# Optimization experiments

Hardware: AMD Instinct MI355X
Metric: run time of the kernel (lower is better)

The kernel has to match this reference:

```python
import jax, jax.numpy as jnp
import numpy as np
import math

B, S, V = 16, 128, 32000
D_MODEL, D_STATE, L, T = 1024, 512, 2, 4
TAU, THR = 2.0, 1.0
DECAY = math.exp(-1.0 / TAU)  # membrane decay exp(-1/tau)
EPS = 1e-5
ALPHA = 2.0  # ATan surrogate alpha


@jax.custom_vjp
def atan_spike(x):
    # spikingjelly surrogate.ATan: heaviside forward, atan-derivative backward
    return (x >= 0.0).astype(x.dtype)

def _atan_fwd(x):
    return atan_spike(x), x

def _atan_bwd(x, g):
    return (g * (ALPHA / 2.0) / (1.0 + (jnp.pi / 2.0 * ALPHA * x) ** 2),)

atan_spike.defvjp(_atan_fwd, _atan_bwd)


def lif(mem, x):
    # AdaptiveLIFNeuron in eval mode: threshold fixed at base_threshold=1.0
    mem_t = mem * DECAY + x
    spike = atan_spike(mem_t - THR)
    return mem_t * (1.0 - spike), spike  # soft-ish reset: mem*(1-spike)


def layernorm(x, g, b):
    m = jnp.mean(x, -1, keepdims=True)
    v = jnp.mean((x - m) ** 2, -1, keepdims=True)
    return (x - m) * jax.lax.rsqrt(v + EPS) * g + b


def setup_inputs() -> dict:
    key = jax.random.key(0)
    ks = jax.random.split(key, 8)

    def w(k, shape, fan_in):
        return (jax.random.normal(k, shape, jnp.float32) / np.sqrt(fan_in).astype(np.float32))

    return {
        "input_ids": jax.random.randint(ks[0], (B, S), 0, V),
        "emb_table": jax.random.normal(ks[1], (V, D_MODEL), jnp.float32) * 0.02,
        "W_enc": w(ks[2], (D_MODEL, D_MODEL), D_MODEL),
        "b_enc": jnp.zeros((D_MODEL,), jnp.float32),
        "ln_s_g": jnp.ones((L, D_STATE), jnp.float32),
        "ln_s_b": jnp.zeros((L, D_STATE), jnp.float32),
        "Wg": w(ks[3], (L, D_STATE, D_MODEL), D_STATE),
        "bg": jnp.zeros((L, D_MODEL), jnp.float32),
        "ln_e_g": jnp.ones((L, D_MODEL), jnp.float32),
        "ln_e_b": jnp.zeros((L, D_MODEL), jnp.float32),
        "Wi": w(ks[4], (L, D_MODEL, D_STATE), D_MODEL),
        "bi": jnp.zeros((L, D_STATE), jnp.float32),
        "W_out": w(ks[5], (D_STATE, V), D_STATE),
        "b_out": jnp.zeros((V,), jnp.float32),
    }


def reference(input_ids, emb_table, W_enc, b_enc, ln_s_g, ln_s_b, Wg, bg,
              ln_e_g, ln_e_b, Wi, bi, W_out, b_out):
    token_emb = emb_table[input_ids]           # [B,S,D_MODEL]
    emb_seq = jnp.swapaxes(token_emb, 0, 1)    # [S,B,D_MODEL]

    init = (
        jnp.zeros((L, B, D_STATE), jnp.float32),  # top-down states per layer
        jnp.zeros((B, D_MODEL), jnp.float32),      # input-encoder LIF mem
        jnp.zeros((L, B, D_MODEL), jnp.float32),   # generative LIF mems
        jnp.zeros((L, B, D_STATE), jnp.float32),   # inference LIF mems
    )

    def token_step(carry, emb_t):
        states, enc_mem, gen_mems, inf_mems = carry
        # input encoder: Linear + LIF; bottom_up_input is the spike output
        enc_mem, bottom = lif(enc_mem, emb_t @ W_enc + b_enc)
        for _t in range(T):
            for j in range(L):
                s = states[j]
                # generative pathway: prediction from top-down state
                pre = layernorm(s, ln_s_g[j], ln_s_b[j]) @ Wg[j] + bg[j]
                gm, pred = lif(gen_mems[j], pre)
                gen_mems = gen_mems.at[j].set(gm)
                error = bottom - pred
                # inference pathway: state update from prediction error
                inf_in = layernorm(error, ln_e_g[j], ln_e_b[j]) @ Wi[j] + bi[j]
                im, upd = lif(inf_mems[j], inf_in)
                inf_mems = inf_mems.at[j].set(im)
                states = states.at[j].set(s + upd)
                bottom = error  # error propagates upward / across timesteps
        return (states, enc_mem, gen_mems, inf_mems), states[L - 1]

    _, hs = jax.lax.scan(token_step, init, emb_seq)  # [S,B,D_STATE]
    hs = jnp.swapaxes(hs, 0, 1)                      # [B,S,D_STATE]
    return hs @ W_out + b_out                        # logits [B,S,V]
```

## Files before the change

kernel.cpp:

```cpp
#include <hip/hip_runtime.h>
#include <math.h>

#define NWG 256
#define TPB 256

typedef float v4f __attribute__((ext_vector_type(4)));

constexpr int Bn = 16, Sn = 128, Vn = 32000, DMn = 1024, DSn = 512;
constexpr float DECAYc = 0.6065306597126334f;
constexpr float THRc = 1.0f, EPSc = 1e-5f;

constexpr size_t OF_FLAGS  = 0;
constexpr size_t OF_STATES = (size_t)256*4096;
constexpr size_t OF_E0     = OF_STATES + (size_t)2*16*512*4;
constexpr size_t OF_E1     = OF_E0 + (size_t)16*1024*4;
constexpr size_t OF_ENCX   = OF_E1 + (size_t)16*1024*4;
constexpr size_t OF_HS     = OF_ENCX + (size_t)128*16*1024*4;
constexpr size_t OF_WGT    = OF_HS + (size_t)128*16*512*4;
constexpr size_t OF_WIT    = OF_WGT + (size_t)2*1024*512*4;
constexpr size_t INIT_BYTES = OF_E0;

struct SP {
  const int* ids; const float* emb;
  const float* W_enc; const float* b_enc;
  const float* ln_s_g; const float* ln_s_b;
  const float* Wg; const float* bg;
  const float* ln_e_g; const float* ln_e_b;
  const float* Wi; const float* bi;
};

__device__ __forceinline__ float ld_cg(const float* p) {
  return __hip_atomic_load(p, __ATOMIC_RELAXED, __HIP_MEMORY_SCOPE_AGENT);
}
__device__ __forceinline__ void st_cg(float* p, float v) {
  __hip_atomic_store(p, v, __ATOMIC_RELAXED, __HIP_MEMORY_SCOPE_AGENT);
}
__device__ __forceinline__ int ld_flag(const int* p) {
  return __hip_atomic_load(p, __ATOMIC_RELAXED, __HIP_MEMORY_SCOPE_AGENT);
}
__device__ __forceinline__ void st_flag(int* p, int v) {
  __hip_atomic_store(p, v, __ATOMIC_RELAXED, __HIP_MEMORY_SCOPE_AGENT);
}

__device__ __forceinline__ int swc(int c) { return c ^ ((c >> 3) & 7); }

template<int SZ>
__device__ __forceinline__ void bstep(float* v, bool up, int M) {
  #pragma unroll
  for (int q = 0; q < SZ/2; q++) {
    float lo = v[q], hi = v[q + SZ/2];
    float send = up ? lo : hi;
    float recv = __shfl_xor(send, M);
    v[q] = (up ? hi : lo) + recv;
  }
}

template<int K, int NO, int ROP>
__device__ __forceinline__ void step_fn(
    const float* __restrict__ WT,
    const float* __restrict__ bias,
    const float* __restrict__ lng, const float* __restrict__ lnb,
    const float* __restrict__ src,
    float* __restrict__ mreg, float* __restrict__ btreg, float* __restrict__ streg,
    float* __restrict__ encmem, const float* __restrict__ encrow,
    float* __restrict__ errw, float* __restrict__ stw, float* __restrict__ hsw,
    int o0, int grp, float* X, int tid)
{
  constexpr int Kc = K / 64, KC4 = Kc / 4, OPW = NO / 4, NV = 4 * OPW;
  const int w = tid >> 6, l = tid & 63;
  const int o_i   = (OPW == 8) ? ((l >> 3) & 7) : ((l >> 4) & 3);
  const int b_loc = (OPW == 8) ? ((l >> 1) & 3) : ((l >> 2) & 3);
  const int o  = o0 + w*OPW + o_i;
  const int bg = grp*4 + b_loc;

  float eEv = 0.f;
  if (ROP == 1) {
    const float ex = encrow[(size_t)bg*DMn + o];
    const float emt = encmem[0]*DECAYc + ex;
    const float esp = (emt >= THRc) ? 1.f : 0.f;
    encmem[0] = emt * (1.f - esp);
    eEv = esp;
  }

  float wreg[Kc][OPW];
  #pragma unroll
  for (int i = 0; i < OPW; i++) {
    const v4f* wp = (const v4f*)(WT + (size_t)(o0 + w*OPW + i)*K + l*Kc);
    #pragma unroll
    for (int q = 0; q < KC4; q++) {
      v4f v = wp[q];
      #pragma unroll
      for (int e = 0; e < 4; e++) wreg[q*4 + e][i] = v[e];
    }
  }

  {
    v4f xr[KC4];
    const float* sp = src + (size_t)(grp*4 + w)*K + l*Kc;
    #pragma unroll
    for (int q = 0; q < KC4; q++)
      asm volatile("global_load_dwordx4 %0, %1, off sc0 sc1"
                   : "=v"(xr[q]) : "v"(sp + 4*q));
    asm volatile("s_waitcnt vmcnt(0)" ::: "memory");
    __builtin_amdgcn_sched_barrier(0);
    float s1 = 0.f;
    #pragma unroll
    for (int q = 0; q < KC4; q++)
      #pragma unroll
      for (int e = 0; e < 4; e++) s1 += xr[q][e];
    #pragma unroll
    for (int off = 32; off; off >>= 1) s1 += __shfl_xor(s1, off);
    const float mean = s1 * (1.0f / K);
    float s2 = 0.f;
    #pragma unroll
    for (int q = 0; q < KC4; q++)
      #pragma unroll
      for (int e = 0; e < 4; e++) { float d = xr[q][e] - mean; s2 += d*d; }
    #pragma unroll
    for (int off = 32; off; off >>= 1) s2 += __shfl_xor(s2, off);
    const float rstd = 1.0f / sqrtf(s2 * (1.0f / K) + EPSc);
    #pragma unroll
    for (int q = 0; q < KC4; q++) {
      v4f ov;
      #pragma unroll
      for (int e = 0; e < 4; e++) {
        const int k = l*Kc + q*4 + e;
        ov[e] = (xr[q][e] - mean) * rstd * lng[k] + lnb[k];
      }
      *(v4f*)(X + w*K + (swc(l*KC4 + q) << 2)) = ov;
    }
  }
  __syncthreads();

  int xoff[KC4];
  #pragma unroll
  for (int q = 0; q < KC4; q++) xoff[q] = swc(l*KC4 + q) << 2;
  float v[NV];
  #pragma unroll
  for (int n = 0; n < NV; n++) v[n] = 0.f;
  #pragma unroll
  for (int b = 0; b < 4; b++) {
    v4f xv[KC4];
    #pragma unroll
    for (int q = 0; q < KC4; q++) xv[q] = *(const v4f*)(X + b*K + xoff[q]);
    #pragma unroll
    for (int i = 0; i < OPW; i++) {
      float a = v[i*4 + b];
      #pragma unroll
      for (int q = 0; q < KC4; q++)
        #pragma unroll
        for (int e = 0; e < 4; e++) a = fmaf(xv[q][e], wreg[q*4 + e][i], a);
      v[i*4 + b] = a;
    }
  }

  if (OPW == 8) {
    bstep<32>(v, (l & 32) != 0, 32);
    bstep<16>(v, (l & 16) != 0, 16);
    bstep<8> (v, (l &  8) != 0,  8);
    bstep<4> (v, (l &  4) != 0,  4);
    bstep<2> (v, (l &  2) != 0,  2);
    v[0] += __shfl_xor(v[0], 1);
  } else {
    bstep<16>(v, (l & 32) != 0, 32);
    bstep<8> (v, (l & 16) != 0, 16);
    bstep<4> (v, (l &  8) != 0,  8);
    bstep<2> (v, (l &  4) != 0,  4);
    v[0] += __shfl_xor(v[0], 2);
    v[0] += __shfl_xor(v[0], 1);
  }

  const float val = v[0] + bias[o];
  const float mt = mreg[0] * DECAYc + val;
  const float spk = (mt >= THRc) ? 1.f : 0.f;
  mreg[0] = mt * (1.f - spk);
  if (ROP == 1 || ROP == 2) {
    const float ne = ((ROP == 1) ? eEv : btreg[0]) - spk;
    btreg[0] = ne;
    if ((l & 1) == 0) st_cg(errw + (size_t)bg*DMn + o, ne);
  } else {
    const float ns = streg[0] + spk;
    streg[0] = ns;
    if ((l & 3) == 0) {
      st_cg(stw + (size_t)bg*DSn + o, ns);
      if (hsw) hsw[(size_t)bg*DSn + o] = ns;
    }
  }
}

__device__ __forceinline__ void publish(int* myflag, int tid, int epoch) {
  asm volatile("s_waitcnt vmcnt(0)" ::: "memory");
  __syncthreads();
  if (tid == 0) st_flag(myflag, epoch);
}
__device__ __forceinline__ void waithalf(const int* othf, int tid, int target) {
  if (tid < 32) {
    while (ld_flag(othf + tid*1024) < target) { }
  }
  asm volatile("" ::: "memory");
  __syncthreads();
}

__global__ void __launch_bounds__(TPB, 1) snn_scan(SP p, char* __restrict__ ws)
{
  __shared__ float X[21504];
  const int wgg = blockIdx.x, tid = threadIdx.x;
  const int grp = wgg >> 6, wgl = wgg & 63;
  int* flags  = (int*)(ws + OF_FLAGS);
  int* myflag = flags + (size_t)wgg*1024;
  float* states = (float*)(ws + OF_STATES);
  float* e0     = (float*)(ws + OF_E0);
  float* e1     = (float*)(ws + OF_E1);
  const float* encX = (const float*)(ws + OF_ENCX);
  float* hs     = (float*)(ws + OF_HS);
  const float* WgT = (const float*)(ws + OF_WGT);
  const float* WiT = (const float*)(ws + OF_WIT);
  float* ebuf[2] = { e0, e1 };

  if (wgl < 32) {
    const int* othf = flags + (size_t)(grp*64 + 32)*1024;
    float encMem = 0.f, btReg = 0.f, genMem0 = 0.f, genMem1 = 0.f;
    const int o0 = wgl * 32;
    for (int s = 0; s < Sn; s++) {
      for (int it = 0; it < 8; it++) {
        const int j = it & 1;
        waithalf(othf, tid, s*8 + it - 1);
        if (it == 0)
          step_fn<512,32,1>(WgT, p.bg, p.ln_s_g, p.ln_s_b, states,
                            &genMem0, &btReg, nullptr,
                            &encMem, encX + (size_t)s*Bn*DMn,
                            ebuf[0], nullptr, nullptr, o0, grp, X, tid);
        else
          step_fn<512,32,2>(WgT + (size_t)j*DMn*DSn, p.bg + j*DMn,
                            p.ln_s_g + j*DSn, p.ln_s_b + j*DSn,
                            states + (size_t)j*Bn*DSn,
                            j ? &genMem1 : &genMem0, &btReg, nullptr,
                            nullptr, nullptr,
                            ebuf[j], nullptr, nullptr, o0, grp, X, tid);
        publish(myflag, tid, s*8 + it + 1);
      }
    }
  } else {
    const int* othf = flags + (size_t)(grp*64)*1024;
    float infMem0 = 0.f, infMem1 = 0.f, stReg0 = 0.f, stReg1 = 0.f;
    const int o0 = (wgl - 32) * 16;
    for (int s = 0; s < Sn; s++) {
      for (int it = 0; it < 8; it++) {
        const int j = it & 1;
        waithalf(othf, tid, s*8 + it + 1);
        step_fn<1024,16,3>(WiT + (size_t)j*DSn*DMn, p.bi + j*DSn,
                           p.ln_e_g + j*DMn, p.ln_e_b + j*DMn,
                           ebuf[j],
                           j ? &infMem1 : &infMem0, nullptr,
                           j ? &stReg1 : &stReg0,
                           nullptr, nullptr,
                           nullptr, states + (size_t)j*Bn*DSn,
                           (it == 7) ? (hs + (size_t)s*Bn*DSn) : nullptr,
                           o0, grp, X, tid);
        publish(myflag, tid, s*8 + it + 1);
      }
    }
  }
}

__global__ void __launch_bounds__(256) transpose_k(
    const float* __restrict__ in, float* __restrict__ out, int K, int O)
{
  __shared__ float t[32][33];
  const int ob = blockIdx.x * 32, kb = blockIdx.y * 32;
  const int x = threadIdx.x, y = threadIdx.y;
  #pragma unroll
  for (int i = 0; i < 32; i += 8) t[y + i][x] = in[(size_t)(kb + y + i)*O + ob + x];
  __syncthreads();
  #pragma unroll
  for (int i = 0; i < 32; i += 8) out[(size_t)(ob + y + i)*K + kb + x] = t[x][y + i];
}

__global__ void __launch_bounds__(256) enc_gemm(
    const int* __restrict__ ids, const float* __restrict__ emb,
    const float* __restrict__ We, const float* __restrict__ be,
    float* __restrict__ encX)
{
  __shared__ float As[32][128];
  __shared__ float Bs[32][128];
  __shared__ int rowid[128];
  const int tid = threadIdx.x;
  const int ntile = blockIdx.x * 128;
  const int mtile = blockIdx.y * 128;
  if (tid < 128) {
    int m = mtile + tid;
    rowid[tid] = ids[(m & 15)*Sn + (m >> 4)];
  }
  __syncthreads();
  const int tx = tid & 15, ty = tid >> 4;
  float acc[8][8];
  #pragma unroll
  for (int i = 0; i < 8; i++)
    #pragma unroll
    for (int q = 0; q < 8; q++) acc[i][q] = 0.f;

  for (int kb = 0; kb < 32; kb++) {
    #pragma unroll
    for (int r = 0; r < 4; r++) {
      int idx = tid + r*256;
      int m = idx >> 3, kq = idx & 7;
      float4 a = *(const float4*)(emb + (size_t)rowid[m]*DMn + kb*32 + kq*4);
      As[kq*4+0][m] = a.x; As[kq*4+1][m] = a.y;
      As[kq*4+2][m] = a.z; As[kq*4+3][m] = a.w;
    }
    #pragma unroll
    for (int r = 0; r < 4; r++) {
      int idx = tid + r*256;
      int k = idx >> 5, nq = idx & 31;
      *(float4*)(&Bs[k][nq*4]) =
          *(const float4*)(We + (size_t)(kb*32 + k)*DMn + ntile + nq*4);
    }
    __syncthreads();
    #pragma unroll
    for (int k = 0; k < 32; k++) {
      float4 a0 = *(float4*)(&As[k][ty*8]);
      float4 a1 = *(float4*)(&As[k][ty*8+4]);
      float4 b0 = *(float4*)(&Bs[k][tx*8]);
      float4 b1 = *(float4*)(&Bs[k][tx*8+4]);
      float av[8] = {a0.x,a0.y,a0.z,a0.w,a1.x,a1.y,a1.z,a1.w};
      float bv[8] = {b0.x,b0.y,b0.z,b0.w,b1.x,b1.y,b1.z,b1.w};
      #pragma unroll
      for (int i = 0; i < 8; i++)
        #pragma unroll
        for (int q = 0; q < 8; q++) acc[i][q] += av[i]*bv[q];
    }
    __syncthreads();
  }
  const float* bop = be + ntile + tx*8;
  float4 bv0 = *(const float4*)bop;
  float4 bv1 = *(const float4*)(bop + 4);
  #pragma unroll
  for (int i = 0; i < 8; i++) {
    int m = mtile + ty*8 + i;
    float* op = encX + (size_t)m*DMn + ntile + tx*8;
    float4 v0 = make_float4(acc[i][0]+bv0.x, acc[i][1]+bv0.y,
                            acc[i][2]+bv0.z, acc[i][3]+bv0.w);
    float4 v1 = make_float4(acc[i][4]+bv1.x, acc[i][5]+bv1.y,
                            acc[i][6]+bv1.z, acc[i][7]+bv1.w);
    *(float4*)op = v0;
    *(float4*)(op + 4) = v1;
  }
}

__global__ void __launch_bounds__(256) out_gemm(
    const float* __restrict__ hs, const float* __restrict__ Wo,
    const float* __restrict__ bo, float* __restrict__ out)
{
  __shared__ float As[32][128];
  __shared__ float Bs[32][128];
  const int tid = threadIdx.x;
  const int ntile = blockIdx.x * 128;
  const int mtile = blockIdx.y * 128;
  const int tx = tid & 15, ty = tid >> 4;
  float acc[8][8];
  #pragma unroll
  for (int i = 0; i < 8; i++)
    #pragma unroll
    for (int q = 0; q < 8; q++) acc[i][q] = 0.f;

  for (int kb = 0; kb < 16; kb++) {
    #pragma unroll
    for (int r = 0; r < 4; r++) {
      int idx = tid + r*256;
      int m = idx >> 3, kq = idx & 7;
      float4 a = *(const float4*)(hs + (size_t)(mtile + m)*512 + kb*32 + kq*4);
      As[kq*4+0][m] = a.x; As[kq*4+1][m] = a.y;
      As[kq*4+2][m] = a.z; As[kq*4+3][m] = a.w;
    }
    #pragma unroll
    for (int r = 0; r < 4; r++) {
      int idx = tid + r*256;
      int k = idx >> 5, nq = idx & 31;
      *(float4*)(&Bs[k][nq*4]) =
          *(const float4*)(Wo + (size_t)(kb*32 + k)*Vn + ntile + nq*4);
    }
    __syncthreads();
    #pragma unroll
    for (int k = 0; k < 32; k++) {
      float4 a0 = *(float4*)(&As[k][ty*8]);
      float4 a1 = *(float4*)(&As[k][ty*8+4]);
      float4 b0 = *(float4*)(&Bs[k][tx*8]);
      float4 b1 = *(float4*)(&Bs[k][tx*8+4]);
      float av[8] = {a0.x,a0.y,a0.z,a0.w,a1.x,a1.y,a1.z,a1.w};
      float bv[8] = {b0.x,b0.y,b0.z,b0.w,b1.x,b1.y,b1.z,b1.w};
      #pragma unroll
      for (int i = 0; i < 8; i++)
        #pragma unroll
        for (int q = 0; q < 8; q++) acc[i][q] += av[i]*bv[q];
    }
    __syncthreads();
  }
  const float* bop = bo + ntile + tx*8;
  float4 bv0 = *(const float4*)bop;
  float4 bv1 = *(const float4*)(bop + 4);
  #pragma unroll
  for (int i = 0; i < 8; i++) {
    int m = mtile + ty*8 + i;
    float* op = out + ((size_t)(m & 15)*Sn + (m >> 4))*Vn + ntile + tx*8;
    float4 v0 = make_float4(acc[i][0]+bv0.x, acc[i][1]+bv0.y,
                            acc[i][2]+bv0.z, acc[i][3]+bv0.w);
    float4 v1 = make_float4(acc[i][4]+bv1.x, acc[i][5]+bv1.y,
                            acc[i][6]+bv1.z, acc[i][7]+bv1.w);
    *(float4*)op = v0;
    *(float4*)(op + 4) = v1;
  }
}

extern "C" void kernel_launch(void* const* d_in, const int* in_sizes, int n_in,
                              void* d_out, int out_size, void* d_ws, size_t ws_size,
                              hipStream_t stream) {
  (void)in_sizes; (void)n_in; (void)out_size; (void)ws_size;
  SP p;
  p.ids    = (const int*)  d_in[0];
  p.emb    = (const float*)d_in[1];
  p.W_enc  = (const float*)d_in[2];
  p.b_enc  = (const float*)d_in[3];
  p.ln_s_g = (const float*)d_in[4];
  p.ln_s_b = (const float*)d_in[5];
  p.Wg     = (const float*)d_in[6];
  p.bg     = (const float*)d_in[7];
  p.ln_e_g = (const float*)d_in[8];
  p.ln_e_b = (const float*)d_in[9];
  p.Wi     = (const float*)d_in[10];
  p.bi     = (const float*)d_in[11];
  const float* Wo = (const float*)d_in[12];
  const float* bo = (const float*)d_in[13];

  char* ws = (char*)d_ws;
  float* WgT  = (float*)(ws + OF_WGT);
  float* WiT  = (float*)(ws + OF_WIT);
  float* encX = (float*)(ws + OF_ENCX);
  float* hs   = (float*)(ws + OF_HS);

  hipMemsetAsync(ws, 0, INIT_BYTES, stream);

  hipLaunchKernelGGL(transpose_k, dim3(32, 16), dim3(32, 8), 0, stream,
                     p.Wg, WgT, 512, 1024);
  hipLaunchKernelGGL(transpose_k, dim3(32, 16), dim3(32, 8), 0, stream,
                     p.Wg + (size_t)512*1024, WgT + (size_t)1024*512, 512, 1024);
  hipLaunchKernelGGL(transpose_k, dim3(16, 32), dim3(32, 8), 0, stream,
                     p.Wi, WiT, 1024, 512);
  hipLaunchKernelGGL(transpose_k, dim3(16, 32), dim3(32, 8), 0, stream,
                     p.Wi + (size_t)1024*512, WiT + (size_t)512*1024, 1024, 512);

  hipLaunchKernelGGL(enc_gemm, dim3(DMn/128, 2048/128), dim3(256), 0, stream,
                     p.ids, p.emb, p.W_enc, p.b_enc, encX);

  hipLaunchKernelGGL(snn_scan, dim3(NWG), dim3(TPB), 0, stream, p, ws);

  hipLaunchKernelGGL(out_gemm, dim3(Vn/128, 2048/128), dim3(256), 0, stream,
                     hs, Wo, bo, (float*)d_out);
}
```

Baseline: 5.233 ms.

## Keep both layers' weights and layernorm params resident in registers across scan

Before, each step of the persistent scan kernel reloaded its weight slice, layernorm gamma/beta and bias from global memory. Now both layers' slices are loaded once into registers before the sequence loop, and the 8 inner steps are fully unrolled with specialised gen/inf step functions. The aim is to take repeated global weight traffic off the latency-bound serial critical path. The cost is roughly doubled register pressure from holding two layers' weights, which may cause spills. The shared buffer is switched to dynamic allocation of the same size.

```diff
diff --git a/kernel.cpp b/kernel.cpp
--- a/kernel.cpp
+++ b/kernel.cpp
@@ -29,9 +29,6 @@
   const float* Wi; const float* bi;
 };
 
-__device__ __forceinline__ float ld_cg(const float* p) {
-  return __hip_atomic_load(p, __ATOMIC_RELAXED, __HIP_MEMORY_SCOPE_AGENT);
-}
 __device__ __forceinline__ void st_cg(float* p, float v) {
   __hip_atomic_store(p, v, __ATOMIC_RELAXED, __HIP_MEMORY_SCOPE_AGENT);
 }
@@ -55,139 +52,6 @@
   }
 }
 
-template<int K, int NO, int ROP>
-__device__ __forceinline__ void step_fn(
-    const float* __restrict__ WT,
-    const float* __restrict__ bias,
-    const float* __restrict__ lng, const float* __restrict__ lnb,
-    const float* __restrict__ src,
-    float* __restrict__ mreg, float* __restrict__ btreg, float* __restrict__ streg,
-    float* __restrict__ encmem, const float* __restrict__ encrow,
-    float* __restrict__ errw, float* __restrict__ stw, float* __restrict__ hsw,
-    int o0, int grp, float* X, int tid)
-{
-  constexpr int Kc = K / 64, KC4 = Kc / 4, OPW = NO / 4, NV = 4 * OPW;
-  const int w = tid >> 6, l = tid & 63;
-  const int o_i   = (OPW == 8) ? ((l >> 3) & 7) : ((l >> 4) & 3);
-  const int b_loc = (OPW == 8) ? ((l >> 1) & 3) : ((l >> 2) & 3);
-  const int o  = o0 + w*OPW + o_i;
-  const int bg = grp*4 + b_loc;
-
-  float eEv = 0.f;
-  if (ROP == 1) {
-    const float ex = encrow[(size_t)bg*DMn + o];
-    const float emt = encmem[0]*DECAYc + ex;
-    const float esp = (emt >= THRc) ? 1.f : 0.f;
-    encmem[0] = emt * (1.f - esp);
-    eEv = esp;
-  }
-
-  float wreg[Kc][OPW];
-  #pragma unroll
-  for (int i = 0; i < OPW; i++) {
-    const v4f* wp = (const v4f*)(WT + (size_t)(o0 + w*OPW + i)*K + l*Kc);
-    #pragma unroll
-    for (int q = 0; q < KC4; q++) {
-      v4f v = wp[q];
-      #pragma unroll
-      for (int e = 0; e < 4; e++) wreg[q*4 + e][i] = v[e];
-    }
-  }
-
-  {
-    v4f xr[KC4];
-    const float* sp = src + (size_t)(grp*4 + w)*K + l*Kc;
-    #pragma unroll
-    for (int q = 0; q < KC4; q++)
-      asm volatile("global_load_dwordx4 %0, %1, off sc0 sc1"
-                   : "=v"(xr[q]) : "v"(sp + 4*q));
-    asm volatile("s_waitcnt vmcnt(0)" ::: "memory");
-    __builtin_amdgcn_sched_barrier(0);
-    float s1 = 0.f;
-    #pragma unroll
-    for (int q = 0; q < KC4; q++)
-      #pragma unroll
-      for (int e = 0; e < 4; e++) s1 += xr[q][e];
-    #pragma unroll
-    for (int off = 32; off; off >>= 1) s1 += __shfl_xor(s1, off);
-    const float mean = s1 * (1.0f / K);
-    float s2 = 0.f;
-    #pragma unroll
-    for (int q = 0; q < KC4; q++)
-      #pragma unroll
-      for (int e = 0; e < 4; e++) { float d = xr[q][e] - mean; s2 += d*d; }
-    #pragma unroll
-    for (int off = 32; off; off >>= 1) s2 += __shfl_xor(s2, off);
-    const float rstd = 1.0f / sqrtf(s2 * (1.0f / K) + EPSc);
-    #pragma unroll
-    for (int q = 0; q < KC4; q++) {
-      v4f ov;
-      #pragma unroll
-      for (int e = 0; e < 4; e++) {
-        const int k = l*Kc + q*4 + e;
-        ov[e] = (xr[q][e] - mean) * rstd * lng[k] + lnb[k];
-      }
-      *(v4f*)(X + w*K + (swc(l*KC4 + q) << 2)) = ov;
-    }
-  }
-  __syncthreads();
-
-  int xoff[KC4];
-  #pragma unroll
-  for (int q = 0; q < KC4; q++) xoff[q] = swc(l*KC4 + q) << 2;
-  float v[NV];
-  #pragma unroll
-  for (int n = 0; n < NV; n++) v[n] = 0.f;
-  #pragma unroll
-  for (int b = 0; b < 4; b++) {
-    v4f xv[KC4];
-    #pragma unroll
-    for (int q = 0; q < KC4; q++) xv[q] = *(const v4f*)(X + b*K + xoff[q]);
-    #pragma unroll
-    for (int i = 0; i < OPW; i++) {
-      float a = v[i*4 + b];
-      #pragma unroll
-      for (int q = 0; q < KC4; q++)
-        #pragma unroll
-        for (int e = 0; e < 4; e++) a = fmaf(xv[q][e], wreg[q*4 + e][i], a);
-      v[i*4 + b] = a;
-    }
-  }
-
-  if (OPW == 8) {
-    bstep<32>(v, (l & 32) != 0, 32);
-    bstep<16>(v, (l & 16) != 0, 16);
-    bstep<8> (v, (l &  8) != 0,  8);
-    bstep<4> (v, (l &  4) != 0,  4);
-    bstep<2> (v, (l &  2) != 0,  2);
-    v[0] += __shfl_xor(v[0], 1);
-  } else {
-    bstep<16>(v, (l & 32) != 0, 32);
-    bstep<8> (v, (l & 16) != 0, 16);
-    bstep<4> (v, (l &  8) != 0,  8);
-    bstep<2> (v, (l &  4) != 0,  4);
-    v[0] += __shfl_xor(v[0], 2);
-    v[0] += __shfl_xor(v[0], 1);
-  }
-
-  const float val = v[0] + bias[o];
-  const float mt = mreg[0] * DECAYc + val;
-  const float spk = (mt >= THRc) ? 1.f : 0.f;
-  mreg[0] = mt * (1.f - spk);
-  if (ROP == 1 || ROP == 2) {
-    const float ne = ((ROP == 1) ? eEv : btreg[0]) - spk;
-    btreg[0] = ne;
-    if ((l & 1) == 0) st_cg(errw + (size_t)bg*DMn + o, ne);
-  } else {
-    const float ns = streg[0] + spk;
-    streg[0] = ns;
-    if ((l & 3) == 0) {
-      st_cg(stw + (size_t)bg*DSn + o, ns);
-      if (hsw) hsw[(size_t)bg*DSn + o] = ns;
-    }
-  }
-}
-
 __device__ __forceinline__ void publish(int* myflag, int tid, int epoch) {
   asm volatile("s_waitcnt vmcnt(0)" ::: "memory");
   __syncthreads();
@@ -201,11 +65,162 @@
   __syncthreads();
 }
 
+template<bool FIRST>
+__device__ __forceinline__ void gen_step(
+    const float (&wreg)[8][8], const float (&lg)[8], const float (&lb)[8],
+    float biasv, const float* __restrict__ src,
+    float& mreg, float& btReg, float eEv,
+    float* __restrict__ errw, int o, int bg, int grp, float* X, int tid)
+{
+  const int w = tid >> 6, l = tid & 63;
+  v4f xr0, xr1;
+  const float* sp = src + (size_t)(grp*4 + w)*DSn + l*8;
+  asm volatile("global_load_dwordx4 %0, %1, off sc0 sc1" : "=v"(xr0) : "v"(sp));
+  asm volatile("global_load_dwordx4 %0, %1, off sc0 sc1" : "=v"(xr1) : "v"(sp + 4));
+  asm volatile("s_waitcnt vmcnt(0)" ::: "memory");
+  __builtin_amdgcn_sched_barrier(0);
+  float s1 = 0.f;
+  #pragma unroll
+  for (int e = 0; e < 4; e++) { s1 += xr0[e]; s1 += xr1[e]; }
+  #pragma unroll
+  for (int off = 32; off; off >>= 1) s1 += __shfl_xor(s1, off);
+  const float mean = s1 * (1.0f / 512.0f);
+  float s2 = 0.f;
+  #pragma unroll
+  for (int e = 0; e < 4; e++) {
+    float d0 = xr0[e] - mean; s2 += d0*d0;
+    float d1 = xr1[e] - mean; s2 += d1*d1;
+  }
+  #pragma unroll
+  for (int off = 32; off; off >>= 1) s2 += __shfl_xor(s2, off);
+  const float rstd = 1.0f / sqrtf(s2 * (1.0f / 512.0f) + EPSc);
+  v4f ov0, ov1;
+  #pragma unroll
+  for (int e = 0; e < 4; e++) {
+    ov0[e] = (xr0[e] - mean)*rstd*lg[e]   + lb[e];
+    ov1[e] = (xr1[e] - mean)*rstd*lg[4+e] + lb[4+e];
+  }
+  *(v4f*)(X + w*DSn + (swc(l*2 + 0) << 2)) = ov0;
+  *(v4f*)(X + w*DSn + (swc(l*2 + 1) << 2)) = ov1;
+  __syncthreads();
+  const int xo0 = swc(l*2 + 0) << 2, xo1 = swc(l*2 + 1) << 2;
+  float v[32];
+  #pragma unroll
+  for (int n = 0; n < 32; n++) v[n] = 0.f;
+  #pragma unroll
+  for (int b = 0; b < 4; b++) {
+    v4f x0 = *(const v4f*)(X + b*DSn + xo0);
+    v4f x1 = *(const v4f*)(X + b*DSn + xo1);
+    #pragma unroll
+    for (int i = 0; i < 8; i++) {
+      float a = v[i*4 + b];
+      #pragma unroll
+      for (int e = 0; e < 4; e++) a = fmaf(x0[e], wreg[e][i], a);
+      #pragma unroll
+      for (int e = 0; e < 4; e++) a = fmaf(x1[e], wreg[4+e][i], a);
+      v[i*4 + b] = a;
+    }
+  }
+  bstep<32>(v, (l & 32) != 0, 32);
+  bstep<16>(v, (l & 16) != 0, 16);
+  bstep<8> (v, (l &  8) != 0,  8);
+  bstep<4> (v, (l &  4) != 0,  4);
+  bstep<2> (v, (l &  2) != 0,  2);
+  v[0] += __shfl_xor(v[0], 1);
+  const float val = v[0] + biasv;
+  const float mt = mreg * DECAYc + val;
+  const float spk = (mt >= THRc) ? 1.f : 0.f;
+  mreg = mt * (1.f - spk);
+  const float ne = (FIRST ? eEv : btReg) - spk;
+  btReg = ne;
+  if ((l & 1) == 0) st_cg(errw + (size_t)bg*DMn + o, ne);
+}
+
+__device__ __forceinline__ void inf_step(
+    const float (&wreg)[16][4], const float (&lg)[16], const float (&lb)[16],
+    float biasv, const float* __restrict__ src,
+    float& mreg, float& streg,
+    float* __restrict__ stw, float* __restrict__ hsw,
+    int o, int bg, int grp, float* X, int tid)
+{
+  const int w = tid >> 6, l = tid & 63;
+  v4f xr[4];
+  const float* sp = src + (size_t)(grp*4 + w)*DMn + l*16;
+  #pragma unroll
+  for (int q = 0; q < 4; q++)
+    asm volatile("global_load_dwordx4 %0, %1, off sc0 sc1" : "=v"(xr[q]) : "v"(sp + 4*q));
+  asm volatile("s_waitcnt vmcnt(0)" ::: "memory");
+  __builtin_amdgcn_sched_barrier(0);
+  float s1 = 0.f;
+  #pragma unroll
+  for (int q = 0; q < 4; q++)
+    #pragma unroll
+    for (int e = 0; e < 4; e++) s1 += xr[q][e];
+  #pragma unroll
+  for (int off = 32; off; off >>= 1) s1 += __shfl_xor(s1, off);
+  const float mean = s1 * (1.0f / 1024.0f);
+  float s2 = 0.f;
+  #pragma unroll
+  for (int q = 0; q < 4; q++)
+    #pragma unroll
+    for (int e = 0; e < 4; e++) { float d = xr[q][e] - mean; s2 += d*d; }
+  #pragma unroll
+  for (int off = 32; off; off >>= 1) s2 += __shfl_xor(s2, off);
+  const float rstd = 1.0f / sqrtf(s2 * (1.0f / 1024.0f) + EPSc);
+  #pragma unroll
+  for (int q = 0; q < 4; q++) {
+    v4f ov;
+    #pragma unroll
+    for (int e = 0; e < 4; e++)
+      ov[e] = (xr[q][e] - mean)*rstd*lg[q*4+e] + lb[q*4+e];
+    *(v4f*)(X + w*DMn + (swc(l*4 + q) << 2)) = ov;
+  }
+  __syncthreads();
+  int xo[4];
+  #pragma unroll
+  for (int q = 0; q < 4; q++) xo[q] = swc(l*4 + q) << 2;
+  float v[16];
+  #pragma unroll
+  for (int n = 0; n < 16; n++) v[n] = 0.f;
+  #pragma unroll
+  for (int b = 0; b < 4; b++) {
+    v4f xv[4];
+    #pragma unroll
+    for (int q = 0; q < 4; q++) xv[q] = *(const v4f*)(X + b*DMn + xo[q]);
+    #pragma unroll
+    for (int i = 0; i < 4; i++) {
+      float a = v[i*4 + b];
+      #pragma unroll
+      for (int q = 0; q < 4; q++)
+        #pragma unroll
+        for (int e = 0; e < 4; e++) a = fmaf(xv[q][e], wreg[q*4+e][i], a);
+      v[i*4 + b] = a;
+    }
+  }
+  bstep<16>(v, (l & 32) != 0, 32);
+  bstep<8> (v, (l & 16) != 0, 16);
+  bstep<4> (v, (l &  8) != 0,  8);
+  bstep<2> (v, (l &  4) != 0,  4);
+  v[0] += __shfl_xor(v[0], 2);
+  v[0] += __shfl_xor(v[0], 1);
+  const float val = v[0] + biasv;
+  const float mt = mreg * DECAYc + val;
+  const float spk = (mt >= THRc) ? 1.f : 0.f;
+  mreg = mt * (1.f - spk);
+  const float ns = streg + spk;
+  streg = ns;
+  if ((l & 3) == 0) {
+    st_cg(stw + (size_t)bg*DSn + o, ns);
+    if (hsw) hsw[(size_t)bg*DSn + o] = ns;
+  }
+}
+
 __global__ void __launch_bounds__(TPB, 1) snn_scan(SP p, char* __restrict__ ws)
 {
-  __shared__ float X[21504];
+  extern __shared__ float X[];
   const int wgg = blockIdx.x, tid = threadIdx.x;
   const int grp = wgg >> 6, wgl = wgg & 63;
+  const int w = tid >> 6, l = tid & 63;
   int* flags  = (int*)(ws + OF_FLAGS);
   int* myflag = flags + (size_t)wgg*1024;
   float* states = (float*)(ws + OF_STATES);
@@ -215,50 +230,137 @@
   float* hs     = (float*)(ws + OF_HS);
   const float* WgT = (const float*)(ws + OF_WGT);
   const float* WiT = (const float*)(ws + OF_WIT);
-  float* ebuf[2] = { e0, e1 };
+  float* st0 = states;
+  float* st1 = states + (size_t)Bn*DSn;
 
   if (wgl < 32) {
     const int* othf = flags + (size_t)(grp*64 + 32)*1024;
-    float encMem = 0.f, btReg = 0.f, genMem0 = 0.f, genMem1 = 0.f;
     const int o0 = wgl * 32;
+    const int o_i = (l >> 3) & 7, b_loc = (l >> 1) & 3;
+    const int o = o0 + w*8 + o_i, bg = grp*4 + b_loc;
+    float wA[8][8], wB[8][8];
+    #pragma unroll
+    for (int i = 0; i < 8; i++) {
+      const v4f* pa = (const v4f*)(WgT + (size_t)(o0 + w*8 + i)*DSn + l*8);
+      const v4f* pb = (const v4f*)(WgT + (size_t)DMn*DSn + (size_t)(o0 + w*8 + i)*DSn + l*8);
+      v4f a0 = pa[0], a1 = pa[1], b0 = pb[0], b1 = pb[1];
+      #pragma unroll
+      for (int e = 0; e < 4; e++) {
+        wA[e][i] = a0[e]; wA[4+e][i] = a1[e];
+        wB[e][i] = b0[e]; wB[4+e][i] = b1[e];
+      }
+    }
+    float lgA[8], lbA[8], lgB[8], lbB[8];
+    {
+      const v4f* g0 = (const v4f*)(p.ln_s_g + l*8);
+      const v4f* c0 = (const v4f*)(p.ln_s_b + l*8);
+      const v4f* g1 = (const v4f*)(p.ln_s_g + DSn + l*8);
+      const v4f* c1 = (const v4f*)(p.ln_s_b + DSn + l*8);
+      v4f ga = g0[0], gb = g0[1], ba = c0[0], bb = c0[1];
+      v4f gc = g1[0], gd = g1[1], bc = c1[0], bd = c1[1];
+      #pragma unroll
+      for (int e = 0; e < 4; e++) {
+        lgA[e] = ga[e]; lgA[4+e] = gb[e]; lbA[e] = ba[e]; lbA[4+e] = bb[e];
+        lgB[e] = gc[e]; lgB[4+e] = gd[e]; lbB[e] = bc[e]; lbB[4+e] = bd[e];
+      }
+    }
+    const float biasA = p.bg[o], biasB = p.bg[DMn + o];
+    float encMem = 0.f, btReg = 0.f, genMemA = 0.f, genMemB = 0.f;
+
     for (int s = 0; s < Sn; s++) {
-      for (int it = 0; it < 8; it++) {
-        const int j = it & 1;
-        waithalf(othf, tid, s*8 + it - 1);
-        if (it == 0)
-          step_fn<512,32,1>(WgT, p.bg, p.ln_s_g, p.ln_s_b, states,
-                            &genMem0, &btReg, nullptr,
-                            &encMem, encX + (size_t)s*Bn*DMn,
-                            ebuf[0], nullptr, nullptr, o0, grp, X, tid);
-        else
-          step_fn<512,32,2>(WgT + (size_t)j*DMn*DSn, p.bg + j*DMn,
-                            p.ln_s_g + j*DSn, p.ln_s_b + j*DSn,
-                            states + (size_t)j*Bn*DSn,
-                            j ? &genMem1 : &genMem0, &btReg, nullptr,
-                            nullptr, nullptr,
-                            ebuf[j], nullptr, nullptr, o0, grp, X, tid);
-        publish(myflag, tid, s*8 + it + 1);
-      }
+      const int s8 = s*8;
+      const float ex = encX[(size_t)s*Bn*DMn + (size_t)bg*DMn + o];
+      const float emt = encMem*DECAYc + ex;
+      const float esp = (emt >= THRc) ? 1.f : 0.f;
+      encMem = emt * (1.f - esp);
+      waithalf(othf, tid, s8 - 1);
+      gen_step<true >(wA, lgA, lbA, biasA, st0, genMemA, btReg, esp, e0, o, bg, grp, X, tid);
+      publish(myflag, tid, s8 + 1);
+      waithalf(othf, tid, s8 + 0);
+      gen_step<false>(wB, lgB, lbB, biasB, st1, genMemB, btReg, 0.f, e1, o, bg, grp, X, tid);
+      publish(myflag, tid, s8 + 2);
+      waithalf(othf, tid, s8 + 1);
+      gen_step<false>(wA, lgA, lbA, biasA, st0, genMemA, btReg, 0.f, e0, o, bg, grp, X, tid);
+      publish(myflag, tid, s8 + 3);
+      waithalf(othf, tid, s8 + 2);
+      gen_step<false>(wB, lgB, lbB, biasB, st1, genMemB, btReg, 0.f, e1, o, bg, grp, X, tid);
+      publish(myflag, tid, s8 + 4);
+      waithalf(othf, tid, s8 + 3);
+      gen_step<false>(wA, lgA, lbA, biasA, st0, genMemA, btReg, 0.f, e0, o, bg, grp, X, tid);
+      publish(myflag, tid, s8 + 5);
+      waithalf(othf, tid, s8 + 4);
+      gen_step<false>(wB, lgB, lbB, biasB, st1, genMemB, btReg, 0.f, e1, o, bg, grp, X, tid);
+      publish(myflag, tid, s8 + 6);
+      waithalf(othf, tid, s8 + 5);
+      gen_step<false>(wA, lgA, lbA, biasA, st0, genMemA, btReg, 0.f, e0, o, bg, grp, X, tid);
+      publish(myflag, tid, s8 + 7);
+      waithalf(othf, tid, s8 + 6);
+      gen_step<false>(wB, lgB, lbB, biasB, st1, genMemB, btReg, 0.f, e1, o, bg, grp, X, tid);
+      publish(myflag, tid, s8 + 8);
     }
   } else {
     const int* othf = flags + (size_t)(grp*64)*1024;
-    float infMem0 = 0.f, infMem1 = 0.f, stReg0 = 0.f, stReg1 = 0.f;
     const int o0 = (wgl - 32) * 16;
+    const int o_i = (l >> 4) & 3, b_loc = (l >> 2) & 3;
+    const int o = o0 + w*4 + o_i, bg = grp*4 + b_loc;
+    float wA[16][4], wB[16][4];
+    #pragma unroll
+    for (int i = 0; i < 4; i++) {
+      const v4f* pa = (const v4f*)(WiT + (size_t)(o0 + w*4 + i)*DMn + l*16);
+      const v4f* pb = (const v4f*)(WiT + (size_t)DSn*DMn + (size_t)(o0 + w*4 + i)*DMn + l*16);
+      #pragma unroll
+      for (int q = 0; q < 4; q++) {
+        v4f a = pa[q], b = pb[q];
+        #pragma unroll
+        for (int e = 0; e < 4; e++) { wA[q*4+e][i] = a[e]; wB[q*4+e][i] = b[e]; }
+      }
+    }
+    float lgA[16], lbA[16], lgB[16], lbB[16];
+    {
+      const v4f* g0 = (const v4f*)(p.ln_e_g + l*16);
+      const v4f* c0 = (const v4f*)(p.ln_e_b + l*16);
+      const v4f* g1 = (const v4f*)(p.ln_e_g + DMn + l*16);
+      const v4f* c1 = (const v4f*)(p.ln_e_b + DMn + l*16);
+      #pragma unroll
+      for (int q = 0; q < 4; q++) {
+        v4f ga = g0[q], ba = c0[q], gb = g1[q], bb = c1[q];
+        #pragma unroll
+        for (int e = 0; e < 4; e++) {
+          lgA[q*4+e] = ga[e]; lbA[q*4+e] = ba[e];
+          lgB[q*4+e] = gb[e]; lbB[q*4+e] = bb[e];
+        }
+      }
+    }
+    const float biasA = p.bi[o], biasB = p.bi[DSn + o];
+    float infMemA = 0.f, infMemB = 0.f, stRegA = 0.f, stRegB = 0.f;
+
     for (int s = 0; s < Sn; s++) {
-      for (int it = 0; it < 8; it++) {
-        const int j = it & 1;
-        waithalf(othf, tid, s*8 + it + 1);
-        step_fn<1024,16,3>(WiT + (size_t)j*DSn*DMn, p.bi + j*DSn,
-                           p.ln_e_g + j*DMn, p.ln_e_b + j*DMn,
-                           ebuf[j],
-                           j ? &infMem1 : &infMem0, nullptr,
-                           j ? &stReg1 : &stReg0,
-                           nullptr, nullptr,
-                           nullptr, states + (size_t)j*Bn*DSn,
-                           (it == 7) ? (hs + (size_t)s*Bn*DSn) : nullptr,
-                           o0, grp, X, tid);
-        publish(myflag, tid, s*8 + it + 1);
-      }
+      const int s8 = s*8;
+      waithalf(othf, tid, s8 + 1);
+      inf_step(wA, lgA, lbA, biasA, e0, infMemA, stRegA, st0, nullptr, o, bg, grp, X, tid);
+      publish(myflag, tid, s8 + 1);
+      waithalf(othf, tid, s8 + 2);
+      inf_step(wB, lgB, lbB, biasB, e1, infMemB, stRegB, st1, nullptr, o, bg, grp, X, tid);
+      publish(myflag, tid, s8 + 2);
+      waithalf(othf, tid, s8 + 3);
+      inf_step(wA, lgA, lbA, biasA, e0, infMemA, stRegA, st0, nullptr, o, bg, grp, X, tid);
+      publish(myflag, tid, s8 + 3);
+      waithalf(othf, tid, s8 + 4);
+      inf_step(wB, lgB, lbB, biasB, e1, infMemB, stRegB, st1, nullptr, o, bg, grp, X, tid);
+      publish(myflag, tid, s8 + 4);
+      waithalf(othf, tid, s8 + 5);
+      inf_step(wA, lgA, lbA, biasA, e0, infMemA, stRegA, st0, nullptr, o, bg, grp, X, tid);
+      publish(myflag, tid, s8 + 5);
+      waithalf(othf, tid, s8 + 6);
+      inf_step(wB, lgB, lbB, biasB, e1, infMemB, stRegB, st1, nullptr, o, bg, grp, X, tid);
+      publish(myflag, tid, s8 + 6);
+      waithalf(othf, tid, s8 + 7);
+      inf_step(wA, lgA, lbA, biasA, e0, infMemA, stRegA, st0, nullptr, o, bg, grp, X, tid);
+      publish(myflag, tid, s8 + 7);
+      waithalf(othf, tid, s8 + 8);
+      inf_step(wB, lgB, lbB, biasB, e1, infMemB, stRegB, st1,
+               hs + (size_t)s*Bn*DSn, o, bg, grp, X, tid);
+      publish(myflag, tid, s8 + 8);
     }
   }
 }
@@ -451,7 +553,7 @@
   hipLaunchKernelGGL(enc_gemm, dim3(DMn/128, 2048/128), dim3(256), 0, stream,
                      p.ids, p.emb, p.W_enc, p.b_enc, encX);
 
-  hipLaunchKernelGGL(snn_scan, dim3(NWG), dim3(TPB), 0, stream, p, ws);
+  hipLaunchKernelGGL(snn_scan, dim3(NWG), dim3(TPB), 86016, stream, p, ws);
 
   hipLaunchKernelGGL(out_gemm, dim3(Vn/128, 2048/128), dim3(256), 0, stream,
                      hs, Wo, bo, (float*)d_out);
```

Result: faster. 4.528 ms (-13.5%).
